# Performance work log

Measured on AMD Instinct MI355X. Metric: run time of the kernel, lower is better.

Reference implementation:

```python
import jax, jax.numpy as jnp
import numpy as np
import math

D = 512
H = 8
DH = D // H
B, T = 4, 2048


def _poly(x, coeffs):
    # iterative-power polynomial eval, same products as the Vandermonde matmul
    acc = coeffs[0] * jnp.ones_like(x)
    p = jnp.ones_like(x)
    for i in range(1, coeffs.shape[0]):
        p = p * x
        acc = acc + coeffs[i] * p
    return acc


def _exp_fn(x, exp_c):
    return jnp.maximum(_poly(x, exp_c), 1e-8)


def _softmax(x, exp_c):
    x = x - jnp.max(x, axis=-1, keepdims=True)
    e = _exp_fn(x, exp_c)
    return e / jnp.sum(e, axis=-1, keepdims=True)


def _gelu(x, gelu_c):
    return _poly(jnp.clip(x, -4.0, 4.0), gelu_c)


def _layernorm(x, gamma, beta):
    mean = jnp.mean(x, axis=-1, keepdims=True)
    var = jnp.mean(x * x, axis=-1, keepdims=True) - mean * mean
    v = var + 1e-5
    y = jnp.full_like(v, 0.5)
    for _ in range(3):  # Newton iterations for rsqrt
        y = y * (3.0 - v * y * y) * 0.5
    return (x - mean) * y * gamma + beta


def setup_inputs() -> dict:
    key = jax.random.key(0)
    ks = jax.random.split(key, 8)
    x = jax.random.normal(ks[0], (B, T, D), dtype=jnp.float32)
    s = 0.02
    Wq = jax.random.normal(ks[1], (D, D), dtype=jnp.float32) * s
    Wk = jax.random.normal(ks[2], (D, D), dtype=jnp.float32) * s
    Wv = jax.random.normal(ks[3], (D, D), dtype=jnp.float32) * s
    Wo = jax.random.normal(ks[4], (D, D), dtype=jnp.float32) * s
    W1 = jax.random.normal(ks[5], (D, 4 * D), dtype=jnp.float32) * s
    W2 = jax.random.normal(ks[6], (4 * D, D), dtype=jnp.float32) * s
    g1 = jnp.ones((D,), jnp.float32); b1 = jnp.zeros((D,), jnp.float32)
    g2 = jnp.ones((D,), jnp.float32); b2 = jnp.zeros((D,), jnp.float32)
    # GELU degree-7 least-squares fit on [-4,4]
    x_fit = jnp.linspace(-4.0, 4.0, 1000)
    y_fit = 0.5 * x_fit * (1.0 + jax.scipy.special.erf(x_fit / math.sqrt(2.0)))
    V = x_fit[:, None] ** jnp.arange(8)[None, :]
    gelu_c = jnp.linalg.lstsq(V, y_fit)[0].astype(jnp.float32)
    # exp Taylor coeffs degree 6
    exp_c = jnp.array([1.0 / math.factorial(i) for i in range(7)], dtype=jnp.float32)
    return dict(x=x, Wq=Wq, Wk=Wk, Wv=Wv, Wo=Wo, W1=W1, W2=W2,
                g1=g1, b1=b1, g2=g2, b2=b2, gelu_c=gelu_c, exp_c=exp_c)


def reference(x, Wq, Wk, Wv, Wo, W1, W2, g1, b1, g2, b2, gelu_c, exp_c):
    Bn, Tn, Dn = x.shape
    q = (x @ Wq).reshape(Bn, Tn, H, DH).transpose(0, 2, 1, 3)  # [B,H,T,dh]
    k = (x @ Wk).reshape(Bn, Tn, H, DH).transpose(0, 2, 1, 3)
    v = (x @ Wv).reshape(Bn, Tn, H, DH).transpose(0, 2, 1, 3)
    scores = jnp.einsum('bhqd,bhkd->bhqk', q, k) / math.sqrt(DH)
    attn = _softmax(scores, exp_c)
    out = jnp.einsum('bhqk,bhkd->bhqd', attn, v).transpose(0, 2, 1, 3).reshape(Bn, Tn, Dn)
    out = out @ Wo
    h = _layernorm(x + out, g1, b1)
    ffn = _gelu(h @ W1, gelu_c) @ W2
    return _layernorm(h + ffn, g2, b2)
```

## Files before the change

### kernel.cpp

```cpp
#include <hip/hip_runtime.h>
#include <hip/hip_bf16.h>

typedef __bf16 bf16_t;
typedef __bf16 bf16x8 __attribute__((ext_vector_type(8)));
typedef float f32x4 __attribute__((ext_vector_type(4)));

#define MFMA16(a, b, c) __builtin_amdgcn_mfma_f32_16x16x32_bf16((a), (b), (c), 0, 0, 0)

__device__ __forceinline__ void gl_lds16(const bf16_t* g, bf16_t* l) {
  __builtin_amdgcn_global_load_lds(
      (const __attribute__((address_space(1))) void*)g,
      (__attribute__((address_space(3))) void*)l, 16, 0, 0);
}

__device__ __forceinline__ unsigned pack_bf16(float a, float b) {
  union { bf16_t h[2]; unsigned u; } c;
  c.h[0] = (bf16_t)a; c.h[1] = (bf16_t)b;
  return c.u;
}

__global__ __launch_bounds__(256) void k_prep(
    const float* __restrict__ x, bf16_t* __restrict__ x_bf,
    const float* __restrict__ Wq, const float* __restrict__ Wk,
    const float* __restrict__ Wv, const float* __restrict__ Wo,
    const float* __restrict__ W1, const float* __restrict__ W2,
    bf16_t* __restrict__ WqkvT, bf16_t* __restrict__ WoT,
    bf16_t* __restrict__ W1T, bf16_t* __restrict__ W2T) {
  __shared__ float tile[64][65];
  int bid = blockIdx.x, tid = threadIdx.x;
  if (bid < 4096) {
    int i = bid * 256 + tid;
    float4 f = ((const float4*)x)[i];
    union { bf16_t h[4]; uint2 u; } cv;
    cv.h[0] = (bf16_t)f.x; cv.h[1] = (bf16_t)f.y;
    cv.h[2] = (bf16_t)f.z; cv.h[3] = (bf16_t)f.w;
    ((uint2*)x_bf)[i] = cv.u;
    return;
  }
  int t = bid - 4096;
  const float* W; bf16_t* WT; int K, N, idx, gx;
  if (t < 64)       { W = Wq; WT = WqkvT;                      K = 512;  N = 512;  idx = t;       gx = 8;  }
  else if (t < 128) { W = Wk; WT = WqkvT + (size_t)512 * 512;  K = 512;  N = 512;  idx = t - 64;  gx = 8;  }
  else if (t < 192) { W = Wv; WT = WqkvT + (size_t)1024 * 512; K = 512;  N = 512;  idx = t - 128; gx = 8;  }
  else if (t < 256) { W = Wo; WT = WoT;                        K = 512;  N = 512;  idx = t - 192; gx = 8;  }
  else if (t < 512) { W = W1; WT = W1T;                        K = 512;  N = 2048; idx = t - 256; gx = 8;  }
  else              { W = W2; WT = W2T;                        K = 2048; N = 512;  idx = t - 512; gx = 32; }
  int bk = (idx % gx) * 64, bn = (idx / gx) * 64;
  int tx = tid & 63, ty = tid >> 6;
  for (int i = ty; i < 64; i += 4)
    tile[i][tx] = W[(size_t)(bk + i) * N + bn + tx];
  __syncthreads();
  for (int i = ty; i < 64; i += 4)
    WT[(size_t)(bn + i) * K + bk + tx] = (bf16_t)tile[tx][i];
}

template <int MODE, int BM>
__global__ __launch_bounds__(256) void k_gemm_bt(
    const bf16_t* __restrict__ A, const bf16_t* __restrict__ Bt,
    float* __restrict__ Cf, bf16_t* __restrict__ Cb,
    bf16_t* __restrict__ Cb2, bf16_t* __restrict__ Cb3,
    int M, int N, int K, const float* __restrict__ coef) {
  __shared__ __align__(16) bf16_t As[2][BM * 32];
  __shared__ __align__(16) bf16_t Bs[2][128 * 32];
  constexpr int NF = (BM == 128) ? 4 : 2;
  int tid = threadIdx.x;
  int lane = tid & 63, wave = tid >> 6;
  int bm = blockIdx.x * BM, bn = blockIdx.y * 128;
  int wr = (BM == 128) ? (wave >> 1) * 64 : 0;
  int wc = (BM == 128) ? (wave & 1) * 64 : wave * 32;
  int lr = lane & 15, lk = (lane >> 4) * 8;
  int srow = tid >> 2, scol = (tid & 3) * 8;

  f32x4 zero = {0.f, 0.f, 0.f, 0.f};
  f32x4 acc[4][NF];
#pragma unroll
  for (int m = 0; m < 4; ++m)
#pragma unroll
    for (int n = 0; n < NF; ++n) acc[m][n] = zero;

  const bf16_t* pA = A + (size_t)(bm + srow) * K + scol;
  const bf16_t* pB = Bt + (size_t)(bn + srow) * K + scol;

  auto STAGE = [&](int buf, int k0) {
    bf16_t* lA = &As[buf][tid * 8];
    bf16_t* lB = &Bs[buf][tid * 8];
    gl_lds16(pA + k0, lA);
    if (BM == 128) gl_lds16(pA + (size_t)64 * K + k0, lA + 2048);
    gl_lds16(pB + k0, lB);
    gl_lds16(pB + (size_t)64 * K + k0, lB + 2048);
  };

  STAGE(0, 0);
  __syncthreads();
  int buf = 0;
  for (int k0 = 0; k0 < K; k0 += 32) {
    if (k0 + 32 < K) STAGE(buf ^ 1, k0 + 32);
    bf16x8 a[4], b[NF];
#pragma unroll
    for (int m = 0; m < 4; ++m) a[m] = *(const bf16x8*)&As[buf][(wr + m * 16 + lr) * 32 + lk];
#pragma unroll
    for (int n = 0; n < NF; ++n) b[n] = *(const bf16x8*)&Bs[buf][(wc + n * 16 + lr) * 32 + lk];
    __builtin_amdgcn_s_setprio(1);
#pragma unroll
    for (int m = 0; m < 4; ++m)
#pragma unroll
      for (int n = 0; n < NF; ++n)
        acc[m][n] = MFMA16(a[m], b[n], acc[m][n]);
    __builtin_amdgcn_s_setprio(0);
    __syncthreads();
    buf ^= 1;
  }

  float c8[8];
  if (MODE == 4) {
#pragma unroll
    for (int i = 0; i < 8; ++i) c8[i] = coef[i];
  }
  int rbase = (lane >> 4) * 4;
#pragma unroll
  for (int m = 0; m < 4; ++m) {
#pragma unroll
    for (int n = 0; n < NF; ++n) {
#pragma unroll
      for (int r = 0; r < 4; ++r) {
        int gm = bm + wr + m * 16 + rbase + r;
        int gn = bn + wc + n * 16 + lr;
        float v = acc[m][n][r];
        if (MODE == 0) {
          Cf[(size_t)gm * N + gn] = v;
        } else if (MODE == 4) {
          float xx = fminf(fmaxf(v, -4.f), 4.f);
          float p = c8[0], pw = 1.f;
#pragma unroll
          for (int i = 1; i < 8; ++i) { pw *= xx; p += c8[i] * pw; }
          Cb[(size_t)gm * N + gn] = (bf16_t)p;
        } else {
          int mat = gn >> 9, col = gn & 511;
          int b_ = gm >> 11, t_ = gm & 2047, h_ = col >> 6, d_ = col & 63;
          if (mat == 0) {
            Cb[(((size_t)b_ * 8 + h_) * 2048 + t_) * 64 + d_] = (bf16_t)(v * 0.125f);
          } else if (mat == 1) {
            int dsw = d_ ^ ((t_ & 7) << 3);
            Cb2[(((size_t)b_ * 8 + h_) * 2048 + t_) * 64 + dsw] = (bf16_t)v;
          } else {
            int tw = t_ & 63;
            int j = (((tw >> 2) & 3) << 1) | ((tw >> 4) & 1);
            int phys = (((tw & 32) << 1) + (j << 3) + ((tw & 3) << 1)) ^ ((d_ & 7) << 4);
            size_t e = ((((size_t)b_ * 8 + h_) * 64 + d_) * 4096 +
                        (size_t)(t_ >> 6) * 128 + phys) >> 1;
            Cb3[e] = (bf16_t)v;
          }
        }
      }
    }
  }
}

__global__ __launch_bounds__(256) void k_attn(
    const bf16_t* __restrict__ qb, const bf16_t* __restrict__ kb,
    const bf16_t* __restrict__ vtb, bf16_t* __restrict__ ob,
    const float* __restrict__ exp_c) {
  __shared__ __align__(16) bf16_t Ks[3][64 * 64];
  __shared__ __align__(16) bf16_t Vs[2][64 * 64];
  int tid = threadIdx.x, lane = tid & 63, wave = tid >> 6;
  int b0 = blockIdx.x;
  int bid = (b0 & 7) * 64 + (b0 >> 3);
  int qt = bid & 15, bh = bid >> 4;
  const size_t bho = (size_t)bh * (2048 * 64);
  const bf16_t* Q = qb + bho + (size_t)qt * 128 * 64;
  const bf16_t* Kp = kb + bho;
  const bf16_t* Vp = vtb + bho;
  int lr = lane & 15, lg = lane >> 4;

  bf16x8 qa[2][2];
#pragma unroll
  for (int j = 0; j < 2; ++j)
#pragma unroll
    for (int h = 0; h < 2; ++h)
      qa[j][h] = *(const bf16x8*)&Q[(wave * 32 + j * 16 + lr) * 64 + h * 32 + lg * 8];

  float ec[7];
#pragma unroll
  for (int i = 0; i < 7; ++i) ec[i] = exp_c[i];

  union { unsigned u[4]; bf16x8 v; } ones;
#pragma unroll
  for (int i = 0; i < 4; ++i) ones.u[i] = 0x3f803f80u;

  int offA[4], offB[4];
#pragma unroll
  for (int n = 0; n < 4; ++n) {
    int row = n * 16 + lr, sw = (row & 7) << 4;
    offA[n] = (row * 128 + lg * 16) ^ sw;
    offB[n] = (row * 128 + 64 + lg * 16) ^ sw;
  }

  auto STAGE_K = [&](int buf, int kt) {
    bf16_t* lk = &Ks[buf][tid * 8];
    const bf16_t* gk = Kp + (size_t)kt * 4096 + tid * 8;
    gl_lds16(gk, lk);
    gl_lds16(gk + 2048, lk + 2048);
  };
  auto STAGE_V = [&](int buf, int kt) {
    bf16_t* lv = &Vs[buf][tid * 8];
    const bf16_t* gv = Vp + (size_t)(tid >> 3) * 2048 + kt * 64 + (tid & 7) * 8;
    gl_lds16(gv, lv);
    gl_lds16(gv + (size_t)32 * 2048, lv + 2048);
  };

  f32x4 zero = {0.f, 0.f, 0.f, 0.f};
  auto qk_tile = [&](const char* kbase, f32x4 (*sout)[4]) {
    __builtin_amdgcn_s_setprio(1);
#pragma unroll
    for (int n = 0; n < 4; ++n) {
      bf16x8 kb0 = *(const bf16x8*)(kbase + offA[n]);
      bf16x8 kb1 = *(const bf16x8*)(kbase + offB[n]);
#pragma unroll
      for (int j = 0; j < 2; ++j)
        sout[j][n] = MFMA16(kb1, qa[j][1], MFMA16(kb0, qa[j][0], zero));
    }
    __builtin_amdgcn_s_setprio(0);
  };

  f32x4 oacc[2][4], oacc_s[2];
#pragma unroll
  for (int j = 0; j < 2; ++j) {
#pragma unroll
    for (int n = 0; n < 4; ++n) oacc[j][n] = zero;
    oacc_s[j] = zero;
  }

  f32x4 sA[2][4], sB[2][4];

  STAGE_K(0, 0);
  STAGE_K(1, 1);
  STAGE_V(0, 0);
  __syncthreads();
  qk_tile((const char*)Ks[0], sA);

  auto STEP = [&](int kt, f32x4 (*scur)[4], f32x4 (*snext)[4]) {
    if (kt < 30) STAGE_K((kt + 2) % 3, kt + 2);
    if (kt < 31) STAGE_V((kt + 1) & 1, kt + 1);
    if (kt < 31) qk_tile((const char*)Ks[(kt + 1) % 3], snext);
    union { unsigned u[4]; bf16x8 v; } pa[2][2];
#pragma unroll
    for (int j = 0; j < 2; ++j) {
      unsigned pk[4][2];
#pragma unroll
      for (int n = 0; n < 4; ++n) {
        float pf[4];
#pragma unroll
        for (int r = 0; r < 4; ++r) {
          float xv = scur[j][n][r];
          float p = ec[6];
#pragma unroll
          for (int i = 5; i >= 0; --i) p = __builtin_fmaf(p, xv, ec[i]);
          pf[r] = p;
        }
        pk[n][0] = pack_bf16(pf[0], pf[1]);
        pk[n][1] = pack_bf16(pf[2], pf[3]);
      }
      pa[j][0].u[0] = pk[0][0]; pa[j][0].u[1] = pk[0][1];
      pa[j][0].u[2] = pk[1][0]; pa[j][0].u[3] = pk[1][1];
      pa[j][1].u[0] = pk[2][0]; pa[j][1].u[1] = pk[2][1];
      pa[j][1].u[2] = pk[3][0]; pa[j][1].u[3] = pk[3][1];
    }
    const char* vbase = (const char*)Vs[kt & 1];
    __builtin_amdgcn_s_setprio(1);
#pragma unroll
    for (int dd = 0; dd < 4; ++dd) {
      bf16x8 v0 = *(const bf16x8*)(vbase + offA[dd]);
      bf16x8 v1 = *(const bf16x8*)(vbase + offB[dd]);
#pragma unroll
      for (int j = 0; j < 2; ++j)
        oacc[j][dd] = MFMA16(pa[j][1].v, v1, MFMA16(pa[j][0].v, v0, oacc[j][dd]));
    }
#pragma unroll
    for (int j = 0; j < 2; ++j)
      oacc_s[j] = MFMA16(pa[j][1].v, ones.v, MFMA16(pa[j][0].v, ones.v, oacc_s[j]));
    __builtin_amdgcn_s_setprio(0);
    __syncthreads();
  };

  for (int it = 0; it < 16; ++it) {
    STEP(2 * it, sA, sB);
    STEP(2 * it + 1, sB, sA);
  }

  int b_ = bh >> 3, h_ = bh & 7;
#pragma unroll
  for (int j = 0; j < 2; ++j)
#pragma unroll
    for (int dd = 0; dd < 4; ++dd)
#pragma unroll
      for (int r = 0; r < 4; ++r) {
        int t_ = qt * 128 + wave * 32 + j * 16 + lg * 4 + r;
        int d_ = dd * 16 + lr;
        float val = oacc[j][dd][r] / oacc_s[j][r];
        ob[(((size_t)b_ * 2048 + t_) * 8 + h_) * 64 + d_] = (bf16_t)val;
      }
}

__global__ __launch_bounds__(256) void k_ln(
    const float* __restrict__ xa, const float* __restrict__ xb,
    const float* __restrict__ gamma, const float* __restrict__ beta,
    float* __restrict__ outf, bf16_t* __restrict__ outb) {
  int row = blockIdx.x * 4 + (threadIdx.x >> 6);
  int lane = threadIdx.x & 63;
  const float* pa = xa + (size_t)row * 512;
  const float* pb = xb + (size_t)row * 512;
  float4 a0 = ((const float4*)pa)[lane];
  float4 a1 = ((const float4*)pa)[lane + 64];
  float4 b0 = ((const float4*)pb)[lane];
  float4 b1 = ((const float4*)pb)[lane + 64];
  float x[8] = {a0.x + b0.x, a0.y + b0.y, a0.z + b0.z, a0.w + b0.w,
                a1.x + b1.x, a1.y + b1.y, a1.z + b1.z, a1.w + b1.w};
  float s = 0.f, sq = 0.f;
#pragma unroll
  for (int i = 0; i < 8; ++i) { s += x[i]; sq += x[i] * x[i]; }
#pragma unroll
  for (int off = 1; off < 64; off <<= 1) {
    s += __shfl_xor(s, off);
    sq += __shfl_xor(sq, off);
  }
  float mean = s * (1.f / 512.f);
  float var = sq * (1.f / 512.f) - mean * mean;
  float v = var + 1e-5f;
  float y = 0.5f;
#pragma unroll
  for (int it = 0; it < 3; ++it) y = y * (3.0f - v * y * y) * 0.5f;

  float4 g0 = ((const float4*)gamma)[lane];
  float4 g1 = ((const float4*)gamma)[lane + 64];
  float4 e0 = ((const float4*)beta)[lane];
  float4 e1 = ((const float4*)beta)[lane + 64];
  float o[8];
  o[0] = (x[0] - mean) * y * g0.x + e0.x;
  o[1] = (x[1] - mean) * y * g0.y + e0.y;
  o[2] = (x[2] - mean) * y * g0.z + e0.z;
  o[3] = (x[3] - mean) * y * g0.w + e0.w;
  o[4] = (x[4] - mean) * y * g1.x + e1.x;
  o[5] = (x[5] - mean) * y * g1.y + e1.y;
  o[6] = (x[6] - mean) * y * g1.z + e1.z;
  o[7] = (x[7] - mean) * y * g1.w + e1.w;
  float* po = outf + (size_t)row * 512;
  ((float4*)po)[lane]      = make_float4(o[0], o[1], o[2], o[3]);
  ((float4*)po)[lane + 64] = make_float4(o[4], o[5], o[6], o[7]);
  if (outb) {
    bf16_t* pq = outb + (size_t)row * 512;
    union { bf16_t h[4]; uint2 u; } c0, c1;
    c0.h[0] = (bf16_t)o[0]; c0.h[1] = (bf16_t)o[1]; c0.h[2] = (bf16_t)o[2]; c0.h[3] = (bf16_t)o[3];
    c1.h[0] = (bf16_t)o[4]; c1.h[1] = (bf16_t)o[5]; c1.h[2] = (bf16_t)o[6]; c1.h[3] = (bf16_t)o[7];
    ((uint2*)pq)[lane]      = c0.u;
    ((uint2*)pq)[lane + 64] = c1.u;
  }
}

extern "C" void kernel_launch(void* const* d_in, const int* in_sizes, int n_in,
                              void* d_out, int out_size, void* d_ws, size_t ws_size,
                              hipStream_t stream) {
  const float* x      = (const float*)d_in[0];
  const float* Wq     = (const float*)d_in[1];
  const float* Wk     = (const float*)d_in[2];
  const float* Wv     = (const float*)d_in[3];
  const float* Wo     = (const float*)d_in[4];
  const float* W1     = (const float*)d_in[5];
  const float* W2     = (const float*)d_in[6];
  const float* g1     = (const float*)d_in[7];
  const float* b1     = (const float*)d_in[8];
  const float* g2     = (const float*)d_in[9];
  const float* b2     = (const float*)d_in[10];
  const float* gelu_c = (const float*)d_in[11];
  const float* exp_c  = (const float*)d_in[12];

  const int M = 8192;
  const size_t actBF = (size_t)M * 512 * 2;
  char* p = (char*)d_ws;
  auto carve = [&](size_t bytes) {
    void* r = (void*)p;
    p += (bytes + 255) & ~(size_t)255;
    return r;
  };
  bf16_t* x_bf   = (bf16_t*)carve(actBF);
  bf16_t* q_bf   = (bf16_t*)carve(actBF);
  bf16_t* k_bf   = (bf16_t*)carve(actBF);
  bf16_t* vT_bf  = (bf16_t*)carve(actBF);
  bf16_t* o_bf   = (bf16_t*)carve(actBF);
  bf16_t* h_bf   = (bf16_t*)carve(actBF);
  bf16_t* WqkvT  = (bf16_t*)carve((size_t)1536 * 512 * 2);
  bf16_t* WoT    = (bf16_t*)carve(512 * 512 * 2);
  bf16_t* W1T    = (bf16_t*)carve(512 * 2048 * 2);
  bf16_t* W2T    = (bf16_t*)carve(512 * 2048 * 2);
  bf16_t* g_bf   = (bf16_t*)carve((size_t)M * 2048 * 2);
  float*  proj   = (float*)carve((size_t)M * 512 * 4);
  float*  h_f    = (float*)carve((size_t)M * 512 * 4);
  float*  f2     = proj;

  k_prep<<<4864, 256, 0, stream>>>(x, x_bf, Wq, Wk, Wv, Wo, W1, W2,
                                   WqkvT, WoT, W1T, W2T);

  k_gemm_bt<5, 128><<<dim3(64, 12), 256, 0, stream>>>(
      x_bf, WqkvT, nullptr, q_bf, k_bf, vT_bf, M, 1536, 512, nullptr);

  k_attn<<<512, 256, 0, stream>>>(q_bf, k_bf, vT_bf, o_bf, exp_c);

  k_gemm_bt<0, 64><<<dim3(128, 4), 256, 0, stream>>>(
      o_bf, WoT, proj, nullptr, nullptr, nullptr, M, 512, 512, nullptr);

  k_ln<<<2048, 256, 0, stream>>>(x, proj, g1, b1, h_f, h_bf);

  k_gemm_bt<4, 128><<<dim3(64, 16), 256, 0, stream>>>(
      h_bf, W1T, nullptr, g_bf, nullptr, nullptr, M, 2048, 512, gelu_c);

  k_gemm_bt<0, 64><<<dim3(128, 4), 256, 0, stream>>>(
      g_bf, W2T, f2, nullptr, nullptr, nullptr, M, 512, 2048, nullptr);

  k_ln<<<2048, 256, 0, stream>>>(h_f, f2, g2, b2, (float*)d_out, nullptr);
}
```

Before: 191.7 us.

## Split attention over key dimension into two halves with a combine kernel

The attention kernel now splits the 32 key tiles into two halves, launching twice as many blocks. Each block writes unnormalized fp32 partial outputs and row sums into scratch buffers that reuse the g_bf and proj memory. A new combine kernel adds the two partials and divides by the summed row sum to produce the bf16 output. The aim is better occupancy across the GPU's compute units, since 512 blocks may underfill the device. In exchange it adds fp32 partial traffic of about 32MB and an extra kernel launch.

Result: slower. 200.2 us (+4.4%).

```diff
diff --git a/kernel.cpp b/kernel.cpp
--- a/kernel.cpp
+++ b/kernel.cpp
@@ -158,14 +158,15 @@
 
 __global__ __launch_bounds__(256) void k_attn(
     const bf16_t* __restrict__ qb, const bf16_t* __restrict__ kb,
-    const bf16_t* __restrict__ vtb, bf16_t* __restrict__ ob,
-    const float* __restrict__ exp_c) {
+    const bf16_t* __restrict__ vtb, float* __restrict__ part,
+    float* __restrict__ rsb, const float* __restrict__ exp_c) {
   __shared__ __align__(16) bf16_t Ks[3][64 * 64];
   __shared__ __align__(16) bf16_t Vs[2][64 * 64];
   int tid = threadIdx.x, lane = tid & 63, wave = tid >> 6;
   int b0 = blockIdx.x;
-  int bid = (b0 & 7) * 64 + (b0 >> 3);
-  int qt = bid & 15, bh = bid >> 4;
+  int bid = (b0 & 7) * 128 + (b0 >> 3);
+  int ks = bid & 1, qt = (bid >> 1) & 15, bh = bid >> 5;
+  int kt0 = ks * 16;
   const size_t bho = (size_t)bh * (2048 * 64);
   const bf16_t* Q = qb + bho + (size_t)qt * 128 * 64;
   const bf16_t* Kp = kb + bho;
@@ -232,16 +233,16 @@
 
   f32x4 sA[2][4], sB[2][4];
 
-  STAGE_K(0, 0);
-  STAGE_K(1, 1);
-  STAGE_V(0, 0);
+  STAGE_K(0, kt0);
+  STAGE_K(1, kt0 + 1);
+  STAGE_V(0, kt0);
   __syncthreads();
   qk_tile((const char*)Ks[0], sA);
 
-  auto STEP = [&](int kt, f32x4 (*scur)[4], f32x4 (*snext)[4]) {
-    if (kt < 30) STAGE_K((kt + 2) % 3, kt + 2);
-    if (kt < 31) STAGE_V((kt + 1) & 1, kt + 1);
-    if (kt < 31) qk_tile((const char*)Ks[(kt + 1) % 3], snext);
+  auto STEP = [&](int lt, f32x4 (*scur)[4], f32x4 (*snext)[4]) {
+    if (lt < 14) STAGE_K((lt + 2) % 3, kt0 + lt + 2);
+    if (lt < 15) STAGE_V((lt + 1) & 1, kt0 + lt + 1);
+    if (lt < 15) qk_tile((const char*)Ks[(lt + 1) % 3], snext);
     union { unsigned u[4]; bf16x8 v; } pa[2][2];
 #pragma unroll
     for (int j = 0; j < 2; ++j) {
@@ -265,7 +266,7 @@
       pa[j][1].u[0] = pk[2][0]; pa[j][1].u[1] = pk[2][1];
       pa[j][1].u[2] = pk[3][0]; pa[j][1].u[3] = pk[3][1];
     }
-    const char* vbase = (const char*)Vs[kt & 1];
+    const char* vbase = (const char*)Vs[lt & 1];
     __builtin_amdgcn_s_setprio(1);
 #pragma unroll
     for (int dd = 0; dd < 4; ++dd) {
@@ -282,23 +283,47 @@
     __syncthreads();
   };
 
-  for (int it = 0; it < 16; ++it) {
+  for (int it = 0; it < 8; ++it) {
     STEP(2 * it, sA, sB);
     STEP(2 * it + 1, sB, sA);
   }
 
+  float* pp = part + (size_t)ks * (8192 * 512);
   int b_ = bh >> 3, h_ = bh & 7;
 #pragma unroll
-  for (int j = 0; j < 2; ++j)
+  for (int j = 0; j < 2; ++j) {
 #pragma unroll
     for (int dd = 0; dd < 4; ++dd)
 #pragma unroll
       for (int r = 0; r < 4; ++r) {
         int t_ = qt * 128 + wave * 32 + j * 16 + lg * 4 + r;
         int d_ = dd * 16 + lr;
-        float val = oacc[j][dd][r] / oacc_s[j][r];
-        ob[(((size_t)b_ * 2048 + t_) * 8 + h_) * 64 + d_] = (bf16_t)val;
+        pp[(((size_t)b_ * 2048 + t_) * 8 + h_) * 64 + d_] = oacc[j][dd][r];
       }
+    if (lr == 0) {
+#pragma unroll
+      for (int r = 0; r < 4; ++r) {
+        int t_ = qt * 128 + wave * 32 + j * 16 + lg * 4 + r;
+        rsb[ks * 65536 + ((b_ * 2048 + t_) * 8 + h_)] = oacc_s[j][r];
+      }
+    }
+  }
+}
+
+__global__ __launch_bounds__(256) void k_combine(
+    const float* __restrict__ part, const float* __restrict__ rsb,
+    bf16_t* __restrict__ ob) {
+  int gid = blockIdx.x * 256 + threadIdx.x;
+  int row = gid >> 4;
+  float r = rsb[row] + rsb[65536 + row];
+  float4 a = ((const float4*)part)[gid];
+  float4 b = ((const float4*)(part + (size_t)8192 * 512))[gid];
+  union { bf16_t h[4]; uint2 u; } cv;
+  cv.h[0] = (bf16_t)((a.x + b.x) / r);
+  cv.h[1] = (bf16_t)((a.y + b.y) / r);
+  cv.h[2] = (bf16_t)((a.z + b.z) / r);
+  cv.h[3] = (bf16_t)((a.w + b.w) / r);
+  ((uint2*)ob)[gid] = cv.u;
 }
 
 __global__ __launch_bounds__(256) void k_ln(
@@ -395,6 +420,8 @@
   float*  proj   = (float*)carve((size_t)M * 512 * 4);
   float*  h_f    = (float*)carve((size_t)M * 512 * 4);
   float*  f2     = proj;
+  float*  part   = (float*)g_bf;
+  float*  rsb    = (float*)proj;
 
   k_prep<<<4864, 256, 0, stream>>>(x, x_bf, Wq, Wk, Wv, Wo, W1, W2,
                                    WqkvT, WoT, W1T, W2T);
@@ -402,7 +429,9 @@
   k_gemm_bt<5, 128><<<dim3(64, 12), 256, 0, stream>>>(
       x_bf, WqkvT, nullptr, q_bf, k_bf, vT_bf, M, 1536, 512, nullptr);
 
-  k_attn<<<512, 256, 0, stream>>>(q_bf, k_bf, vT_bf, o_bf, exp_c);
+  k_attn<<<1024, 256, 0, stream>>>(q_bf, k_bf, vT_bf, part, rsb, exp_c);
+
+  k_combine<<<4096, 256, 0, stream>>>(part, rsb, o_bf);
 
   k_gemm_bt<0, 64><<<dim3(128, 4), 256, 0, stream>>>(
       o_bf, WoT, proj, nullptr, nullptr, nullptr, M, 512, 512, nullptr);
```
